# Kernel tuning notes

Measured on AMD Instinct MI355X. Metric: run time of the kernel, lower is better.

Reference implementation:

```python
import jax, jax.numpy as jnp
import numpy as np

HID, H, HD, K, L = 512, 8, 64, 64, 767  # hidden, heads, head_dim, clip, coord length
B, S = 2, L + 1  # add_cls pads one token


def _rel_indices(coords, k):
    # torch.cdist p=2: pairwise euclidean distances [B, L, L]
    diff = coords[:, :, None, :] - coords[:, None, :, :]
    dist = jnp.sqrt(jnp.sum(diff * diff, axis=-1))
    # rank along rows / columns via double argsort
    t1 = jnp.argsort(jnp.argsort(dist, axis=-1), axis=-1)
    t2 = jnp.argsort(jnp.argsort(dist, axis=-2), axis=-2)
    nm = jnp.triu(t1, k=1) + jnp.tril(t2, k=1)
    nm = jnp.clip(nm, 0, k)
    # add_cls: prepend a zero column then a zero row -> [B, L+1, L+1]
    nm = jnp.pad(nm, ((0, 0), (1, 0), (1, 0)))
    return nm.astype(jnp.int32)


def setup_inputs() -> dict:
    key = jax.random.key(0)
    ks = jax.random.split(key, 16)
    sc = 0.05
    return {
        "query": jax.random.normal(ks[0], (B, S, HID), jnp.float32),
        "key": jax.random.normal(ks[1], (B, S, HID), jnp.float32),
        "value": jax.random.normal(ks[2], (B, S, HID), jnp.float32),
        "coords": jax.random.normal(ks[3], (B, L, 2), jnp.float32),
        "Wq": jax.random.normal(ks[4], (H, HID, HD), jnp.float32) * sc,
        "bq": jax.random.normal(ks[5], (H, HD), jnp.float32) * sc,
        "Wk": jax.random.normal(ks[6], (H, HID, HD), jnp.float32) * sc,
        "bk": jax.random.normal(ks[7], (H, HD), jnp.float32) * sc,
        "Wv": jax.random.normal(ks[8], (H, HID, HD), jnp.float32) * sc,
        "bv": jax.random.normal(ks[9], (H, HD), jnp.float32) * sc,
        "pe_k": jax.random.normal(ks[10], (K + 1, HD), jnp.float32) * sc,
        "pe_v": jax.random.normal(ks[11], (K + 1, HD), jnp.float32) * sc,
        "fc_W": jax.random.normal(ks[12], (HID, HID), jnp.float32) * sc,
        "fc_b": jax.random.normal(ks[13], (HID,), jnp.float32) * sc,
    }


def reference(query, key, value, coords, Wq, bq, Wk, bk, Wv, bv, pe_k, pe_v, fc_W, fc_b):
    idx = _rel_indices(coords, K)                 # [B, S, S] int
    k_bias = pe_k[idx]                            # [B, S, S, HD]
    v_bias = pe_v[idx]                            # [B, S, S, HD]

    # per-head projections, heads stacked on axis n
    q = jnp.einsum('bsh,nhd->bnsd', query, Wq) + bq[None, :, None, :]
    k = jnp.einsum('bsh,nhd->bnsd', key, Wk) + bk[None, :, None, :]
    v = jnp.einsum('bsh,nhd->bnsd', value, Wv) + bv[None, :, None, :]

    attn1 = jnp.einsum('bnqd,bnkd->bnqk', q, k)
    attn2 = jnp.einsum('bnqd,bqkd->bnqk', q, k_bias)  # per-query relative key bias
    att = jax.nn.softmax((attn1 + attn2) / (HD ** 0.5), axis=-1)

    out1 = jnp.einsum('bnqk,bnkd->bnqd', att, v)
    out2 = jnp.einsum('bnqk,bqkd->bnqd', att, v_bias)  # relative value bias
    heads = (out1 + out2).transpose(0, 2, 1, 3).reshape(B, S, H * HD)  # concat heads
    return heads @ fc_W.T + fc_b
```

## Files before the change

### kernel.cpp

```cpp
#include <hip/hip_runtime.h>
#include <math.h>

#define HIDD 512
#define NH 8
#define HD 64
#define KCLIP 64
#define LCO 767
#define BB 2
#define SS 768

#define TQ 32
#define KT 64
#define NT (SS / KT)
#define KS 4
#define TPB (NT / KS)
#define NROW (BB * NH * SS)
#define QPAD 68

__global__ __launch_bounds__(256) void idx_fill_kernel(int* __restrict__ idx)
{
    size_t gid = (size_t)blockIdx.x * 256 + threadIdx.x;
    size_t base = gid * 4;
    int rem = (int)(base % (size_t)(SS * SS));
    int r = rem / SS, c0 = rem % SS;
    int4 v;
    int* vv = (int*)&v;
#pragma unroll
    for (int u = 0; u < 4; ++u) {
        int c = c0 + u;
        vv[u] = (r == 0 || c == 0 || r == c) ? 0 : KCLIP;
    }
    *(int4*)(idx + base) = v;
}

__global__ __launch_bounds__(256) void rel_idx_kernel(
    const float* __restrict__ coords, int* __restrict__ idx)
{
    __shared__ float cx[LCO], cy[LCO];
    __shared__ unsigned long long dk[LCO];
    __shared__ unsigned long long lst[LCO];
    __shared__ int hist[256];
    __shared__ int cum[256];
    __shared__ int nsel;
    __shared__ int thrB;

    const int blk = blockIdx.x;
    const int b = blk / LCO;
    const int i = blk % LCO;
    const int t = threadIdx.x;
    const float* cb = coords + (size_t)b * LCO * 2;

    hist[t] = 0;
    if (t == 0) nsel = 0;
    for (int j = t; j < LCO; j += 256) {
        float2 c2 = *(const float2*)(cb + 2 * j);
        cx[j] = c2.x; cy[j] = c2.y;
    }
    __syncthreads();
    const float xi = cx[i], yi = cy[i];
    for (int j = t; j < LCO; j += 256) {
        float dx = xi - cx[j];
        float dy = yi - cy[j];
        float d2 = __fadd_rn(__fmul_rn(dx, dx), __fmul_rn(dy, dy));
        float d = sqrtf(d2);
        dk[j] = ((unsigned long long)__float_as_uint(d) << 32) | (unsigned)j;
        int bkt = (int)(d * 32.0f);
        bkt = bkt > 255 ? 255 : bkt;
        atomicAdd(&hist[bkt], 1);
    }
    __syncthreads();

    cum[t] = hist[t];
    __syncthreads();
    for (int off = 1; off < 256; off <<= 1) {
        int add = (t >= off) ? cum[t - off] : 0;
        __syncthreads();
        cum[t] += add;
        __syncthreads();
    }
    if (cum[t] >= KCLIP && (t == 0 || cum[t - 1] < KCLIP)) thrB = t;
    __syncthreads();
    const int B = thrB;

    const int lane = t & 63;
#pragma unroll
    for (int u = 0; u < 3; ++u) {
        int j = t + u * 256;
        bool sel = false;
        unsigned long long key = 0;
        if (j < LCO) {
            key = dk[j];
            float d = __uint_as_float((unsigned)(key >> 32));
            int bkt = (int)(d * 32.0f);
            bkt = bkt > 255 ? 255 : bkt;
            sel = (bkt <= B);
        }
        unsigned long long m = __ballot(sel);
        int base;
        if (lane == 0) base = atomicAdd(&nsel, __popcll(m));
        base = __shfl(base, 0);
        if (sel) {
            int pfx = __popcll(m & ((1ull << lane) - 1));
            lst[base + pfx] = key;
        }
    }
    __syncthreads();
    const int C = nsel;

    int* ib = idx + (size_t)b * SS * SS;
    for (int c = t; c < C; c += 256) {
        unsigned long long myk = lst[c];
        int cnt = 0;
        for (int c2 = 0; c2 < C; ++c2) cnt += (lst[c2] < myk);
        int j = (int)(myk & 0xffffffffu);
        if (cnt < KCLIP && j > i) {
            ib[(size_t)(i + 1) * SS + (j + 1)] = cnt;
            ib[(size_t)(j + 1) * SS + (i + 1)] = cnt;
        }
    }
}

__global__ __launch_bounds__(256) void proj_kernel(
    const float* __restrict__ qin, const float* __restrict__ kin, const float* __restrict__ vin,
    const float* __restrict__ Wq, const float* __restrict__ Wk, const float* __restrict__ Wv,
    const float* __restrict__ bq, const float* __restrict__ bk, const float* __restrict__ bv,
    float* __restrict__ qo, float* __restrict__ kTo, float* __restrict__ vo)
{
    const int z = blockIdx.z;
    const float* A = (z == 0) ? qin : (z == 1) ? kin : vin;
    const float* W = (z == 0) ? Wq : (z == 1) ? Wk : Wv;
    const float* bias = (z == 0) ? bq : (z == 1) ? bk : bv;
    const int h = blockIdx.y;
    const int m0 = blockIdx.x * 64;

    __shared__ float As[32][68];
    __shared__ float Bs[32][64];

    const int t = threadIdx.x;
    const int tx = t & 15, ty = t >> 4;
    const float* Wh = W + (size_t)h * HIDD * HD;

    float acc[4][4] = {};
    for (int k0 = 0; k0 < HIDD; k0 += 32) {
#pragma unroll
        for (int u = 0; u < 2; ++u) {
            int i = t + u * 256;
            int row = i >> 3, kc = (i & 7) * 4;
            float4 a4 = *(const float4*)(A + (size_t)(m0 + row) * HIDD + k0 + kc);
            As[kc + 0][row] = a4.x; As[kc + 1][row] = a4.y;
            As[kc + 2][row] = a4.z; As[kc + 3][row] = a4.w;
            int kr = i >> 4, n4 = (i & 15) * 4;
            *(float4*)(&Bs[kr][n4]) = *(const float4*)(Wh + (size_t)(k0 + kr) * HD + n4);
        }
        __syncthreads();
#pragma unroll
        for (int kk = 0; kk < 32; ++kk) {
            float4 a4 = *(const float4*)(&As[kk][ty * 4]);
            float4 b4 = *(const float4*)(&Bs[kk][tx * 4]);
            float a_[4] = {a4.x, a4.y, a4.z, a4.w};
            float b_[4] = {b4.x, b4.y, b4.z, b4.w};
#pragma unroll
            for (int r = 0; r < 4; ++r)
#pragma unroll
                for (int c = 0; c < 4; ++c) acc[r][c] += a_[r] * b_[c];
        }
        __syncthreads();
    }
#pragma unroll
    for (int r = 0; r < 4; ++r) {
        int m = m0 + ty * 4 + r;
        int bIdx = m / SS, s = m % SS;
#pragma unroll
        for (int c = 0; c < 4; ++c) {
            int d = tx * 4 + c;
            float val = acc[r][c] + bias[h * HD + d];
            if (z == 1) {
                kTo[((size_t)(bIdx * NH + h) * HD + d) * SS + s] = val;
            } else {
                float* O = (z == 0) ? qo : vo;
                O[((size_t)(bIdx * NH + h) * SS + s) * HD + d] = val;
            }
        }
    }
}

__global__ __launch_bounds__(256) void qpk_kernel(
    const float* __restrict__ q, const float* __restrict__ pe_k, float* __restrict__ qpkg)
{
    __shared__ float qs[64][68];
    __shared__ float pk[65][68];
    const int t = threadIdx.x;
    const int q0 = blockIdx.x * 64;
    const int bn = blockIdx.y;
    const float* qbase = q + ((size_t)bn * SS + q0) * HD;
    for (int i = t; i < 64 * 16; i += 256) {
        int row = i >> 4, d4 = (i & 15) * 4;
        *(float4*)(&qs[row][d4]) = *(const float4*)(qbase + (size_t)row * HD + d4);
    }
    for (int i = t; i < 65 * 16; i += 256) {
        int c = i >> 4, d4 = (i & 15) * 4;
        *(float4*)(&pk[c][d4]) = *(const float4*)(pe_k + (size_t)c * HD + d4);
    }
    __syncthreads();
    const int r0 = t >> 2, cg = t & 3;
    float* orow = qpkg + ((size_t)bn * SS + q0 + r0) * QPAD;
    for (int c = cg; c <= KCLIP; c += 4) {
        float acc = 0.f;
#pragma unroll
        for (int d4 = 0; d4 < HD; d4 += 4) {
            float4 qv = *(const float4*)(&qs[r0][d4]);
            float4 pv = *(const float4*)(&pk[c][d4]);
            acc += qv.x * pv.x + qv.y * pv.y + qv.z * pv.z + qv.w * pv.w;
        }
        orow[c] = acc;
    }
}

__global__ __launch_bounds__(256) void attn_part_kernel(
    const float* __restrict__ q, const float* __restrict__ kT,
    const float* __restrict__ vb, const int* __restrict__ idx,
    const float* __restrict__ qpkg,
    float* __restrict__ o1p, float* __restrict__ pspart, float* __restrict__ wbpart)
{
    __shared__ float qsT[HD][TQ];
    __shared__ float kv[KT][HD];
    __shared__ float attQ[TQ][68];
    __shared__ float qpkS[TQ][68];
    __shared__ float wbuf[TQ][KCLIP];

    const int t = threadIdx.x;
    const int bn = blockIdx.y;
    const int b = bn >> 3;
    const int q0 = blockIdx.x * TQ;
    const int ks = blockIdx.z;

    const int qh = t >> 4;
    const int kg = t & 15;

    const float* qbase = q + ((size_t)bn * SS + q0) * HD;
    for (int i = t; i < TQ * 16; i += 256) {
        int r = i >> 4, dx = (i & 15) * 4;
        float4 v4 = *(const float4*)(qbase + (size_t)r * HD + dx);
        qsT[dx + 0][r] = v4.x; qsT[dx + 1][r] = v4.y;
        qsT[dx + 2][r] = v4.z; qsT[dx + 3][r] = v4.w;
    }
    for (int i = t; i < TQ * 17; i += 256) {
        int r = i / 17, c4 = (i % 17) * 4;
        *(float4*)(&qpkS[r][c4]) = *(const float4*)(qpkg + ((size_t)bn * SS + q0 + r) * QPAD + c4);
    }
    for (int i = t; i < TQ * KCLIP; i += 256) ((float*)wbuf)[i] = 0.f;
    __syncthreads();

    const float* kTbn = kT + (size_t)bn * HD * SS;
    const float* vbn = vb + (size_t)bn * SS * HD;
    const int* ib = idx + (size_t)b * SS * SS;

    float out1[2][4] = {};
    float psum[2] = {0.f, 0.f};

    for (int t0 = 0; t0 < TPB; ++t0) {
        const int k0 = (ks * TPB + t0) * KT;
        for (int i = t; i < KT * 16; i += 256) {
            int d = i >> 4, c4 = (i & 15) * 4;
            *(float4*)(&kv[d][c4]) = *(const float4*)(kTbn + (size_t)d * SS + k0 + c4);
        }
        __syncthreads();

        float acc[2][4] = {};
#pragma unroll 16
        for (int d = 0; d < HD; ++d) {
            float q0v = qsT[d][2 * qh];
            float q1v = qsT[d][2 * qh + 1];
            float4 k4 = *(const float4*)(&kv[d][4 * kg]);
            acc[0][0] += q0v * k4.x; acc[0][1] += q0v * k4.y;
            acc[0][2] += q0v * k4.z; acc[0][3] += q0v * k4.w;
            acc[1][0] += q1v * k4.x; acc[1][1] += q1v * k4.y;
            acc[1][2] += q1v * k4.z; acc[1][3] += q1v * k4.w;
        }
#pragma unroll
        for (int e = 0; e < 2; ++e) {
            int qq = 2 * qh + e;
            int4 iv = *(const int4*)(ib + (size_t)(q0 + qq) * SS + k0 + 4 * kg);
            float p0 = expf((acc[e][0] + qpkS[qq][iv.x]) * 0.125f);
            float p1 = expf((acc[e][1] + qpkS[qq][iv.y]) * 0.125f);
            float p2 = expf((acc[e][2] + qpkS[qq][iv.z]) * 0.125f);
            float p3 = expf((acc[e][3] + qpkS[qq][iv.w]) * 0.125f);
            float4 pv4; pv4.x = p0; pv4.y = p1; pv4.z = p2; pv4.w = p3;
            *(float4*)(&attQ[qq][4 * kg]) = pv4;
            if (iv.x < KCLIP) atomicAdd(&wbuf[qq][iv.x], p0);
            if (iv.y < KCLIP) atomicAdd(&wbuf[qq][iv.y], p1);
            if (iv.z < KCLIP) atomicAdd(&wbuf[qq][iv.z], p2);
            if (iv.w < KCLIP) atomicAdd(&wbuf[qq][iv.w], p3);
            psum[e] += p0 + p1 + p2 + p3;
        }
        __syncthreads();

        for (int i = t; i < KT * 16; i += 256) {
            int k = i >> 4, d4 = (i & 15) * 4;
            *(float4*)(&kv[k][d4]) = *(const float4*)(vbn + (size_t)(k0 + k) * HD + d4);
        }
        __syncthreads();

#pragma unroll 16
        for (int k = 0; k < KT; ++k) {
            float a0 = attQ[2 * qh][k];
            float a1 = attQ[2 * qh + 1][k];
            float4 v4 = *(const float4*)(&kv[k][4 * kg]);
            out1[0][0] += a0 * v4.x; out1[0][1] += a0 * v4.y;
            out1[0][2] += a0 * v4.z; out1[0][3] += a0 * v4.w;
            out1[1][0] += a1 * v4.x; out1[1][1] += a1 * v4.y;
            out1[1][2] += a1 * v4.z; out1[1][3] += a1 * v4.w;
        }
        __syncthreads();
    }

#pragma unroll
    for (int off = 8; off; off >>= 1) {
        psum[0] += __shfl_xor(psum[0], off);
        psum[1] += __shfl_xor(psum[1], off);
    }
    const size_t rbase = (size_t)ks * NROW + (size_t)bn * SS + q0;
    if (kg == 0) {
        pspart[rbase + 2 * qh] = psum[0];
        pspart[rbase + 2 * qh + 1] = psum[1];
    }
#pragma unroll
    for (int e = 0; e < 2; ++e) {
        int qq = 2 * qh + e;
        *(float4*)(o1p + (rbase + qq) * HD + 4 * kg) = *(float4*)(out1[e]);
    }
    for (int i = t; i < TQ * KCLIP / 4; i += 256) {
        int r = i >> 4, c4 = (i & 15) * 4;
        *(float4*)(wbpart + (rbase + r) * KCLIP + c4) = *(const float4*)(&wbuf[r][c4]);
    }
}

__global__ __launch_bounds__(256) void attn_combine_kernel(
    const float* __restrict__ o1p, const float* __restrict__ pspart,
    const float* __restrict__ wbpart, const float* __restrict__ pe_v,
    float* __restrict__ heads)
{
    __shared__ float wl[4][66];
    const int t = threadIdx.x;
    const int rt = t >> 6, d = t & 63;
    const int row = blockIdx.x * 4 + rt;
    const int bn = row / SS, qq = row % SS;
    const int b = bn >> 3, n = bn & 7;

    float w = 0.f, rsum = 0.f, o = 0.f;
#pragma unroll
    for (int ks = 0; ks < KS; ++ks) {
        w += wbpart[((size_t)ks * NROW + row) * KCLIP + d];
        rsum += pspart[(size_t)ks * NROW + row];
        o += o1p[((size_t)ks * NROW + row) * HD + d];
    }
    wl[rt][d] = w;
    __syncthreads();

    const float pv64 = pe_v[KCLIP * HD + d];
    float acc = o;
#pragma unroll 8
    for (int c = 0; c < KCLIP; ++c)
        acc += wl[rt][c] * (pe_v[c * HD + d] - pv64);
    heads[((size_t)b * SS + qq) * HIDD + n * HD + d] = acc / rsum + pv64;
}

__global__ __launch_bounds__(256) void fc_kernel(
    const float* __restrict__ heads, const float* __restrict__ fcW,
    const float* __restrict__ fcb, float* __restrict__ out)
{
    const int m0 = blockIdx.x * 32;
    const int n0 = blockIdx.y * 64;

    __shared__ float As[32][36];
    __shared__ float Bs[32][64];

    const int t = threadIdx.x;
    const int ty = t >> 4;
    const int tx = t & 15;

    float acc[2][4] = {};
    for (int k0 = 0; k0 < HIDD; k0 += 32) {
        {
            int row = t >> 3, kc = (t & 7) * 4;
            float4 a4 = *(const float4*)(heads + (size_t)(m0 + row) * HIDD + k0 + kc);
            As[kc + 0][row] = a4.x; As[kc + 1][row] = a4.y;
            As[kc + 2][row] = a4.z; As[kc + 3][row] = a4.w;
        }
#pragma unroll
        for (int u = 0; u < 2; ++u) {
            int i = t + u * 256;
            int nl = i >> 3, kl = (i & 7) * 4;
            float4 bw = *(const float4*)(fcW + (size_t)(n0 + nl) * HIDD + k0 + kl);
            Bs[kl + 0][nl] = bw.x; Bs[kl + 1][nl] = bw.y;
            Bs[kl + 2][nl] = bw.z; Bs[kl + 3][nl] = bw.w;
        }
        __syncthreads();
#pragma unroll
        for (int kk = 0; kk < 32; ++kk) {
            float a0 = As[kk][2 * ty];
            float a1 = As[kk][2 * ty + 1];
            float4 b4 = *(const float4*)(&Bs[kk][4 * tx]);
            acc[0][0] += a0 * b4.x; acc[0][1] += a0 * b4.y;
            acc[0][2] += a0 * b4.z; acc[0][3] += a0 * b4.w;
            acc[1][0] += a1 * b4.x; acc[1][1] += a1 * b4.y;
            acc[1][2] += a1 * b4.z; acc[1][3] += a1 * b4.w;
        }
        __syncthreads();
    }
    float4 bb = *(const float4*)(fcb + n0 + 4 * tx);
#pragma unroll
    for (int e = 0; e < 2; ++e) {
        float4 r4;
        r4.x = acc[e][0] + bb.x; r4.y = acc[e][1] + bb.y;
        r4.z = acc[e][2] + bb.z; r4.w = acc[e][3] + bb.w;
        *(float4*)(out + (size_t)(m0 + 2 * ty + e) * HIDD + n0 + 4 * tx) = r4;
    }
}

extern "C" void kernel_launch(void* const* d_in, const int* in_sizes, int n_in,
                              void* d_out, int out_size, void* d_ws, size_t ws_size,
                              hipStream_t stream)
{
    (void)in_sizes; (void)n_in; (void)out_size; (void)ws_size;
    const float* query  = (const float*)d_in[0];
    const float* key_   = (const float*)d_in[1];
    const float* value  = (const float*)d_in[2];
    const float* coords = (const float*)d_in[3];
    const float* Wq = (const float*)d_in[4];
    const float* bq = (const float*)d_in[5];
    const float* Wk = (const float*)d_in[6];
    const float* bk = (const float*)d_in[7];
    const float* Wv = (const float*)d_in[8];
    const float* bv = (const float*)d_in[9];
    const float* pe_k = (const float*)d_in[10];
    const float* pe_v = (const float*)d_in[11];
    const float* fcW  = (const float*)d_in[12];
    const float* fcb  = (const float*)d_in[13];
    float* out = (float*)d_out;

    char* ws = (char*)d_ws;
    size_t off = 0;
    auto alloc = [&](size_t bytes) -> void* {
        void* p = ws + off;
        off += (bytes + 255) & ~(size_t)255;
        return p;
    };
    int*   idx    = (int*)  alloc((size_t)BB * SS * SS * sizeof(int));
    float* qb     = (float*)alloc((size_t)BB * NH * SS * HD * sizeof(float));
    float* kTb    = (float*)alloc((size_t)BB * NH * HD * SS * sizeof(float));
    float* vb     = (float*)alloc((size_t)BB * NH * SS * HD * sizeof(float));
    float* headb  = (float*)alloc((size_t)BB * SS * HIDD * sizeof(float));
    float* qpkg   = (float*)alloc((size_t)NROW * QPAD * sizeof(float));
    float* o1p    = (float*)alloc((size_t)KS * NROW * HD * sizeof(float));
    float* pspart = (float*)alloc((size_t)KS * NROW * sizeof(float));
    float* wbpart = (float*)alloc((size_t)KS * NROW * KCLIP * sizeof(float));

    idx_fill_kernel<<<(BB * SS * SS) / (256 * 4), 256, 0, stream>>>(idx);

    rel_idx_kernel<<<BB * LCO, 256, 0, stream>>>(coords, idx);

    proj_kernel<<<dim3((BB * SS) / 64, NH, 3), 256, 0, stream>>>(
        query, key_, value, Wq, Wk, Wv, bq, bk, bv, qb, kTb, vb);

    qpk_kernel<<<dim3(SS / 64, BB * NH), 256, 0, stream>>>(qb, pe_k, qpkg);

    attn_part_kernel<<<dim3(SS / TQ, BB * NH, KS), 256, 0, stream>>>(
        qb, kTb, vb, idx, qpkg, o1p, pspart, wbpart);

    attn_combine_kernel<<<NROW / 4, 256, 0, stream>>>(o1p, pspart, wbpart, pe_v, headb);

    fc_kernel<<<dim3((BB * SS) / 32, HIDD / 64), 256, 0, stream>>>(headb, fcW, fcb, out);
}
```

Baseline: 247.2 us.

## Split-K projection with atomics, finer qpk tiles, fast exp, wider PV loads

The QKV projection is split four ways along the hidden dimension, which multiplies the block count by four. A new init kernel pre-fills the bias, and the partial products are accumulated with global atomicAdd. The qpk kernel uses 16-query tiles to launch more blocks, the attention softmax switches to __expf, and the PV inner loop reads two attention values at once as float2. In exchange the change adds an extra launch and scattered atomic traffic (the transposed-K writes are strided), and the atomic ordering makes the projection results nondeterministic.

```diff
diff --git a/kernel.cpp b/kernel.cpp
--- a/kernel.cpp
+++ b/kernel.cpp
@@ -16,6 +16,7 @@
 #define TPB (NT / KS)
 #define NROW (BB * NH * SS)
 #define QPAD 68
+#define NPROJ (BB * SS * HIDD)
 
 __global__ __launch_bounds__(256) void idx_fill_kernel(int* __restrict__ idx)
 {
@@ -120,18 +121,42 @@
     }
 }
 
-__global__ __launch_bounds__(256) void proj_kernel(
+__global__ __launch_bounds__(256) void qkv_init_kernel(
+    const float* __restrict__ bq, const float* __restrict__ bk, const float* __restrict__ bv,
+    float* __restrict__ qo, float* __restrict__ kTo, float* __restrict__ vo)
+{
+    const int z = blockIdx.y;
+    size_t base = ((size_t)blockIdx.x * 256 + threadIdx.x) * 4;
+    float4 v;
+    if (z == 1) {
+        int rowT = (int)(base / SS);
+        int h = (rowT >> 6) & 7;
+        int d = rowT & 63;
+        float bb = bk[h * 64 + d];
+        v.x = bb; v.y = bb; v.z = bb; v.w = bb;
+        *(float4*)(kTo + base) = v;
+    } else {
+        int d0 = (int)(base & 63);
+        int row = (int)(base >> 6);
+        int h = (row / SS) & 7;
+        const float* bias = (z == 0) ? bq : bv;
+        v = *(const float4*)(bias + h * 64 + d0);
+        *(float4*)(((z == 0) ? qo : vo) + base) = v;
+    }
+}
+
+__global__ __launch_bounds__(256) void proj_part_kernel(
     const float* __restrict__ qin, const float* __restrict__ kin, const float* __restrict__ vin,
     const float* __restrict__ Wq, const float* __restrict__ Wk, const float* __restrict__ Wv,
-    const float* __restrict__ bq, const float* __restrict__ bk, const float* __restrict__ bv,
     float* __restrict__ qo, float* __restrict__ kTo, float* __restrict__ vo)
 {
-    const int z = blockIdx.z;
+    const int zc = blockIdx.z;
+    const int z = zc >> 2, ksp = zc & 3;
     const float* A = (z == 0) ? qin : (z == 1) ? kin : vin;
     const float* W = (z == 0) ? Wq : (z == 1) ? Wk : Wv;
-    const float* bias = (z == 0) ? bq : (z == 1) ? bk : bv;
     const int h = blockIdx.y;
     const int m0 = blockIdx.x * 64;
+    const int kbase = ksp * 128;
 
     __shared__ float As[32][68];
     __shared__ float Bs[32][64];
@@ -141,7 +166,8 @@
     const float* Wh = W + (size_t)h * HIDD * HD;
 
     float acc[4][4] = {};
-    for (int k0 = 0; k0 < HIDD; k0 += 32) {
+    for (int k0i = 0; k0i < 4; ++k0i) {
+        const int k0 = kbase + k0i * 32;
 #pragma unroll
         for (int u = 0; u < 2; ++u) {
             int i = t + u * 256;
@@ -173,12 +199,11 @@
 #pragma unroll
         for (int c = 0; c < 4; ++c) {
             int d = tx * 4 + c;
-            float val = acc[r][c] + bias[h * HD + d];
             if (z == 1) {
-                kTo[((size_t)(bIdx * NH + h) * HD + d) * SS + s] = val;
+                atomicAdd(&kTo[((size_t)(bIdx * NH + h) * HD + d) * SS + s], acc[r][c]);
             } else {
                 float* O = (z == 0) ? qo : vo;
-                O[((size_t)(bIdx * NH + h) * SS + s) * HD + d] = val;
+                atomicAdd(&O[((size_t)(bIdx * NH + h) * SS + s) * HD + d], acc[r][c]);
             }
         }
     }
@@ -187,14 +212,14 @@
 __global__ __launch_bounds__(256) void qpk_kernel(
     const float* __restrict__ q, const float* __restrict__ pe_k, float* __restrict__ qpkg)
 {
-    __shared__ float qs[64][68];
+    __shared__ float qs[16][68];
     __shared__ float pk[65][68];
     const int t = threadIdx.x;
-    const int q0 = blockIdx.x * 64;
+    const int q0 = blockIdx.x * 16;
     const int bn = blockIdx.y;
     const float* qbase = q + ((size_t)bn * SS + q0) * HD;
-    for (int i = t; i < 64 * 16; i += 256) {
-        int row = i >> 4, d4 = (i & 15) * 4;
+    {
+        int row = t >> 4, d4 = (t & 15) * 4;
         *(float4*)(&qs[row][d4]) = *(const float4*)(qbase + (size_t)row * HD + d4);
     }
     for (int i = t; i < 65 * 16; i += 256) {
@@ -202,13 +227,13 @@
         *(float4*)(&pk[c][d4]) = *(const float4*)(pe_k + (size_t)c * HD + d4);
     }
     __syncthreads();
-    const int r0 = t >> 2, cg = t & 3;
-    float* orow = qpkg + ((size_t)bn * SS + q0 + r0) * QPAD;
-    for (int c = cg; c <= KCLIP; c += 4) {
+    const int qr = t >> 4, cg = t & 15;
+    float* orow = qpkg + ((size_t)bn * SS + q0 + qr) * QPAD;
+    for (int c = cg; c <= KCLIP; c += 16) {
         float acc = 0.f;
 #pragma unroll
         for (int d4 = 0; d4 < HD; d4 += 4) {
-            float4 qv = *(const float4*)(&qs[r0][d4]);
+            float4 qv = *(const float4*)(&qs[qr][d4]);
             float4 pv = *(const float4*)(&pk[c][d4]);
             acc += qv.x * pv.x + qv.y * pv.y + qv.z * pv.z + qv.w * pv.w;
         }
@@ -225,7 +250,7 @@
     __shared__ float qsT[HD][TQ];
     __shared__ float kv[KT][HD];
     __shared__ float attQ[TQ][68];
-    __shared__ float qpkS[TQ][68];
+    __shared__ float qpkS[TQ][QPAD];
     __shared__ float wbuf[TQ][KCLIP];
 
     const int t = threadIdx.x;
@@ -281,10 +306,10 @@
         for (int e = 0; e < 2; ++e) {
             int qq = 2 * qh + e;
             int4 iv = *(const int4*)(ib + (size_t)(q0 + qq) * SS + k0 + 4 * kg);
-            float p0 = expf((acc[e][0] + qpkS[qq][iv.x]) * 0.125f);
-            float p1 = expf((acc[e][1] + qpkS[qq][iv.y]) * 0.125f);
-            float p2 = expf((acc[e][2] + qpkS[qq][iv.z]) * 0.125f);
-            float p3 = expf((acc[e][3] + qpkS[qq][iv.w]) * 0.125f);
+            float p0 = __expf((acc[e][0] + qpkS[qq][iv.x]) * 0.125f);
+            float p1 = __expf((acc[e][1] + qpkS[qq][iv.y]) * 0.125f);
+            float p2 = __expf((acc[e][2] + qpkS[qq][iv.z]) * 0.125f);
+            float p3 = __expf((acc[e][3] + qpkS[qq][iv.w]) * 0.125f);
             float4 pv4; pv4.x = p0; pv4.y = p1; pv4.z = p2; pv4.w = p3;
             *(float4*)(&attQ[qq][4 * kg]) = pv4;
             if (iv.x < KCLIP) atomicAdd(&wbuf[qq][iv.x], p0);
@@ -301,15 +326,20 @@
         }
         __syncthreads();
 
-#pragma unroll 16
-        for (int k = 0; k < KT; ++k) {
-            float a0 = attQ[2 * qh][k];
-            float a1 = attQ[2 * qh + 1][k];
-            float4 v4 = *(const float4*)(&kv[k][4 * kg]);
-            out1[0][0] += a0 * v4.x; out1[0][1] += a0 * v4.y;
-            out1[0][2] += a0 * v4.z; out1[0][3] += a0 * v4.w;
-            out1[1][0] += a1 * v4.x; out1[1][1] += a1 * v4.y;
-            out1[1][2] += a1 * v4.z; out1[1][3] += a1 * v4.w;
+#pragma unroll 8
+        for (int kk = 0; kk < KT; kk += 2) {
+            float2 a0 = *(const float2*)(&attQ[2 * qh][kk]);
+            float2 a1 = *(const float2*)(&attQ[2 * qh + 1][kk]);
+            float4 v0 = *(const float4*)(&kv[kk][4 * kg]);
+            float4 v1 = *(const float4*)(&kv[kk + 1][4 * kg]);
+            out1[0][0] += a0.x * v0.x; out1[0][1] += a0.x * v0.y;
+            out1[0][2] += a0.x * v0.z; out1[0][3] += a0.x * v0.w;
+            out1[1][0] += a1.x * v0.x; out1[1][1] += a1.x * v0.y;
+            out1[1][2] += a1.x * v0.z; out1[1][3] += a1.x * v0.w;
+            out1[0][0] += a0.y * v1.x; out1[0][1] += a0.y * v1.y;
+            out1[0][2] += a0.y * v1.z; out1[0][3] += a0.y * v1.w;
+            out1[1][0] += a1.y * v1.x; out1[1][1] += a1.y * v1.y;
+            out1[1][2] += a1.y * v1.z; out1[1][3] += a1.y * v1.w;
         }
         __syncthreads();
     }
@@ -447,9 +477,9 @@
         return p;
     };
     int*   idx    = (int*)  alloc((size_t)BB * SS * SS * sizeof(int));
-    float* qb     = (float*)alloc((size_t)BB * NH * SS * HD * sizeof(float));
-    float* kTb    = (float*)alloc((size_t)BB * NH * HD * SS * sizeof(float));
-    float* vb     = (float*)alloc((size_t)BB * NH * SS * HD * sizeof(float));
+    float* qb     = (float*)alloc((size_t)NPROJ * sizeof(float));
+    float* kTb    = (float*)alloc((size_t)NPROJ * sizeof(float));
+    float* vb     = (float*)alloc((size_t)NPROJ * sizeof(float));
     float* headb  = (float*)alloc((size_t)BB * SS * HIDD * sizeof(float));
     float* qpkg   = (float*)alloc((size_t)NROW * QPAD * sizeof(float));
     float* o1p    = (float*)alloc((size_t)KS * NROW * HD * sizeof(float));
@@ -460,10 +490,13 @@
 
     rel_idx_kernel<<<BB * LCO, 256, 0, stream>>>(coords, idx);
 
-    proj_kernel<<<dim3((BB * SS) / 64, NH, 3), 256, 0, stream>>>(
-        query, key_, value, Wq, Wk, Wv, bq, bk, bv, qb, kTb, vb);
-
-    qpk_kernel<<<dim3(SS / 64, BB * NH), 256, 0, stream>>>(qb, pe_k, qpkg);
+    qkv_init_kernel<<<dim3(NPROJ / (256 * 4), 3), 256, 0, stream>>>(
+        bq, bk, bv, qb, kTb, vb);
+
+    proj_part_kernel<<<dim3((BB * SS) / 64, NH, 12), 256, 0, stream>>>(
+        query, key_, value, Wq, Wk, Wv, qb, kTb, vb);
+
+    qpk_kernel<<<dim3(SS / 16, BB * NH), 256, 0, stream>>>(qb, pe_k, qpkg);
 
     attn_part_kernel<<<dim3(SS / TQ, BB * NH, KS), 256, 0, stream>>>(
         qb, kTb, vb, idx, qpkg, o1p, pspart, wbpart);
```

Result: slower. 325.3 us (+31.6%).
